# Kernel optimization log

Hardware: AMD Instinct MI355X
Metric: run time of the kernel (lower is better)

The kernel has to match this reference:

```python
import jax, jax.numpy as jnp
import numpy as np

NUM_CLASSES = 19
PROJ_DIM = 128
QUEUE_LEN = 2975
B, H, W = 8, 128, 128
EPS = 1e-12  # torch F.normalize eps


def setup_inputs() -> dict:
    key = jax.random.key(0)
    k0, k1, k2, k3, k4 = jax.random.split(key, 5)
    proj3 = jax.random.normal(k0, (B, PROJ_DIM, H, W), jnp.float32)
    proj4 = jax.random.normal(k1, (B, PROJ_DIM, H, W), jnp.float32)
    proj5 = jax.random.normal(k2, (B, PROJ_DIM, H, W), jnp.float32)
    logits = jax.random.normal(k3, (B, NUM_CLASSES, H, W), jnp.float32)
    q = jax.random.normal(k4, (3, NUM_CLASSES, PROJ_DIM, QUEUE_LEN), jnp.float32)
    # buffers are L2-normalized along proj_dim at init
    queues = q / jnp.maximum(jnp.linalg.norm(q, axis=2, keepdims=True), EPS)
    return {"proj3": proj3, "proj4": proj4, "proj5": proj5,
            "logits": logits, "queues": queues}


def _region_keys(fea, pred):
    """fea: (D, HW) float, pred: (HW,) int. Masked mean per class, L2-normalized."""
    onehot = (pred[None, :] == jnp.arange(NUM_CLASSES)[:, None]).astype(fea.dtype)  # (C, HW)
    counts = onehot.sum(1)                                   # (C,)
    sums = jnp.einsum('ch,dh->cd', onehot, fea)              # (C, D)
    present = counts > 0
    means = sums / jnp.maximum(counts, 1.0)[:, None]
    keys = means / jnp.maximum(jnp.linalg.norm(means, axis=1, keepdims=True), EPS)
    return keys, present


def _contrast_loss(keys, present, queue):
    """keys: (C, D), queue: (C, D, L) (detached in original). Sum over present classes."""
    q = jax.lax.stop_gradient(queue)
    # (query . queue_col) implemented as elementwise-mul + mean over D in the original
    sim = jnp.einsum('cd,kdl->ckl', keys, q) / PROJ_DIM      # (C, C, L)
    ar = jnp.arange(NUM_CLASSES)
    pos = sim[ar, ar, :]                                     # (C, L)  l_pos per class
    exp_all = jnp.exp(sim)
    s_neg = exp_all.sum(axis=(1, 2)) - exp_all[ar, ar, :].sum(1)  # scalar neg mass per class
    loss_c = -(pos - jnp.log(jnp.exp(pos) + s_neg[:, None])).sum(1) / QUEUE_LEN
    return jnp.where(present, loss_c, 0.0).sum()


def _enqueue(queue, ptr, keys, present):
    """Write key into queue column ptr[c] for present classes, advance ptr by 1."""
    ar = jnp.arange(NUM_CLASSES)
    cur = queue[ar, :, ptr]                                  # (C, D)
    newcol = jnp.where(present[:, None], jax.lax.stop_gradient(keys), cur)
    queue = queue.at[ar, :, ptr].set(newcol)
    ptr = jnp.where(present, (ptr + 1) % QUEUE_LEN, ptr)
    return queue, ptr


def reference(proj3, proj4, proj5, logits, queues):
    pred = jnp.argmax(logits, axis=1).reshape(B, -1)         # (B, HW)
    total = jnp.float32(0.0)
    for pi, projector in enumerate((proj3, proj4, proj5)):
        fea_all = projector.reshape(B, PROJ_DIM, -1)          # (B, D, HW)

        def step(carry, inp):
            queue, ptr, acc = carry
            f, p = inp
            keys, present = _region_keys(f, p)
            acc = acc + _contrast_loss(keys, present, queue)
            queue, ptr = _enqueue(queue, ptr, keys, present)
            return (queue, ptr, acc), None

        init = (queues[pi], jnp.zeros((NUM_CLASSES,), jnp.int32), jnp.float32(0.0))
        (_, _, acc), _ = jax.lax.scan(step, init, (fea_all, pred))
        total = total + acc / B
    return total
```

## Files before the change

### kernel.cpp

```cpp
#include <hip/hip_runtime.h>
#include <stdint.h>

#define NCLS 19
#define PDIM 128
#define QLEN 2975
#define BATCH 8
#define HW 16384
#define ROWS 152
#define ROWS_PAD 160
#define HCHUNK 512

typedef __attribute__((ext_vector_type(8))) short short8;
typedef __attribute__((ext_vector_type(4))) float floatx4;

__device__ __forceinline__ uint16_t f2b(float f) {
    uint32_t u = __float_as_uint(f);
    uint32_t r = (u + 0x7FFFu + ((u >> 16) & 1u)) >> 16;
    return (uint16_t)r;
}

__global__ __launch_bounds__(256)
void k_pred(const float* __restrict__ logits, uint8_t* __restrict__ pred,
            int* __restrict__ counts) {
    __shared__ int cnt[NCLS];
    int tid = threadIdx.x;
    if (tid < NCLS) cnt[tid] = 0;
    __syncthreads();
    int idx = blockIdx.x * 256 + tid;
    int b = idx >> 14, h = idx & (HW - 1);
    const float* base = logits + (size_t)b * NCLS * HW + h;
    float best = base[0];
    int bi = 0;
#pragma unroll
    for (int c = 1; c < NCLS; ++c) {
        float v = base[(size_t)c * HW];
        if (v > best) { best = v; bi = c; }
    }
    pred[idx] = (uint8_t)bi;
    atomicAdd(&cnt[bi], 1);
    __syncthreads();
    if (tid < NCLS) atomicAdd(&counts[b * NCLS + tid], cnt[tid]);
}

__global__ __launch_bounds__(512)
void k_msum(const float* __restrict__ p0, const float* __restrict__ p1,
            const float* __restrict__ p2, const uint8_t* __restrict__ pred,
            float* __restrict__ sums) {
    int chunk = blockIdx.x, b = blockIdx.y, pi = blockIdx.z;
    const float* proj = (pi == 0) ? p0 : (pi == 1) ? p1 : p2;
    int tid = threadIdx.x;
    int wave = tid >> 6, lane = tid & 63;
    int col = lane & 15, g = lane >> 4;
    int d = wave * 16 + col;
    int h0 = chunk * HCHUNK;

    const float* frow = proj + ((size_t)b * PDIM + d) * HW + h0;
    const uint8_t* pr = pred + (size_t)b * HW + h0;

    uint4 va[16], vb[16];
    uint64_t pb[16];
#pragma unroll
    for (int s = 0; s < 16; ++s) {
        int hk = s * 32 + g * 8;
        va[s] = *(const uint4*)(frow + hk);
        vb[s] = *(const uint4*)(frow + hk + 4);
        pb[s] = *(const uint64_t*)(pr + hk);
    }
    __builtin_amdgcn_sched_barrier(0);

    floatx4 acc0 = (floatx4)(0.f);
    floatx4 acc1 = (floatx4)(0.f);

#pragma unroll
    for (int s = 0; s < 16; ++s) {
        union { short8 s8; uint32_t w[4]; } bf;
        bf.w[0] = __builtin_amdgcn_perm(va[s].y, va[s].x, 0x07060302u);
        bf.w[1] = __builtin_amdgcn_perm(va[s].w, va[s].z, 0x07060302u);
        bf.w[2] = __builtin_amdgcn_perm(vb[s].y, vb[s].x, 0x07060302u);
        bf.w[3] = __builtin_amdgcn_perm(vb[s].w, vb[s].z, 0x07060302u);

        union { short8 s8; uint16_t h[8]; } a0, a1;
#pragma unroll
        for (int j = 0; j < 8; ++j) {
            int cb = (int)((pb[s] >> (8 * j)) & 0xFF);
            a0.h[j] = (cb == col)      ? (uint16_t)0x3F80 : (uint16_t)0;
            a1.h[j] = (cb == col + 16) ? (uint16_t)0x3F80 : (uint16_t)0;
        }
        acc0 = __builtin_amdgcn_mfma_f32_16x16x32_bf16(a0.s8, bf.s8, acc0, 0, 0, 0);
        acc1 = __builtin_amdgcn_mfma_f32_16x16x32_bf16(a1.s8, bf.s8, acc1, 0, 0, 0);
    }

    float* sb = sums + (((size_t)pi * BATCH + b) * NCLS) * PDIM + d;
#pragma unroll
    for (int r = 0; r < 4; ++r) {
        int row0 = g * 4 + r;
        atomicAdd(&sb[(size_t)row0 * PDIM], acc0[r]);
        int row1 = 16 + g * 4 + r;
        if (row1 < NCLS) atomicAdd(&sb[(size_t)row1 * PDIM], acc1[r]);
    }
}

__global__ __launch_bounds__(64)
void k_keys(const float* __restrict__ sums, const int* __restrict__ counts,
            uint16_t* __restrict__ keysb) {
    int c = blockIdx.x, b = blockIdx.y, pi = blockIdx.z;
    int lane = threadIdx.x;
    size_t base = (((size_t)pi * BATCH + b) * NCLS + c) * PDIM;
    int cn = counts[b * NCLS + c];
    float cnt = (float)(cn > 0 ? cn : 1);
    float m0 = sums[base + lane] / cnt;
    float m1 = sums[base + lane + 64] / cnt;
    float nr = m0 * m0 + m1 * m1;
    for (int off = 32; off; off >>= 1) nr += __shfl_xor(nr, off);
    float scale = 1.f / fmaxf(sqrtf(nr), 1e-12f);
    size_t bb = ((size_t)pi * ROWS_PAD + b * NCLS + c) * PDIM;
    keysb[bb + lane]      = f2b(m0 * scale);
    keysb[bb + lane + 64] = f2b(m1 * scale);
}

__global__ __launch_bounds__(256, 2)
void k_sim(const float* __restrict__ q, const uint16_t* __restrict__ keysb,
           float* __restrict__ Sall, float* __restrict__ D0,
           float* __restrict__ pos0) {
    __shared__ char smem[40960];
    int tile = blockIdx.x, k = blockIdx.y, pi = blockIdx.z;
    int tid = threadIdx.x;
    int wave = tid >> 6, lane = tid & 63;
    int col = lane & 15, g = lane >> 4;

    {
        const uint4* kg = (const uint4*)(keysb + (size_t)pi * ROWS_PAD * PDIM);
        uint4* kl = (uint4*)smem;
        int kgrp = tid & 15;
        int r0 = tid >> 4;
#pragma unroll
        for (int it = 0; it < 10; ++it) {
            int row = r0 + it * 16;
            kl[kgrp * 160 + (row ^ (kgrp & 7))] = kg[row * 16 + kgrp];
        }
    }

    int l0 = tile * 128 + wave * 16 + col;
    int l1 = l0 + 64;
    bool okA = l0 < QLEN, okB = l1 < QLEN;
    const uint32_t* qbase = (const uint32_t*)(q + ((size_t)pi * NCLS + k) * (size_t)PDIM * QLEN);
    const uint32_t* qA = qbase + (okA ? l0 : (QLEN - 1));
    const uint32_t* qB = qbase + (okB ? l1 : (QLEN - 1));

    uint32_t uA[32], uB[32];
#pragma unroll
    for (int s = 0; s < 4; ++s) {
#pragma unroll
        for (int j = 0; j < 8; ++j) {
            size_t off = (size_t)(s * 32 + g * 8 + j) * QLEN;
            uA[s * 8 + j] = qA[off];
            uB[s * 8 + j] = qB[off];
        }
    }

    __syncthreads();

    uint32_t wA[16], wB[16];
#pragma unroll
    for (int t = 0; t < 16; ++t) {
        wA[t] = __builtin_amdgcn_perm(uA[2 * t + 1], uA[2 * t], 0x07060302u);
        wB[t] = __builtin_amdgcn_perm(uB[2 * t + 1], uB[2 * t], 0x07060302u);
    }

    floatx4 accA[10], accB[10];
#pragma unroll
    for (int m = 0; m < 10; ++m) { accA[m] = (floatx4)(0.f); accB[m] = (floatx4)(0.f); }

    const short8* kls = (const short8*)smem;
#pragma unroll
    for (int s = 0; s < 4; ++s) {
        union { short8 s8; uint32_t w[4]; } bfA, bfB;
#pragma unroll
        for (int i = 0; i < 4; ++i) { bfA.w[i] = wA[s * 4 + i]; bfB.w[i] = wB[s * 4 + i]; }
        int kgrp = s * 4 + g;
        int kxor = kgrp & 7;
        const short8* kp = kls + (size_t)kgrp * 160;
#pragma unroll
        for (int m = 0; m < 10; ++m) {
            short8 af = kp[(m * 16 + col) ^ kxor];
            accA[m] = __builtin_amdgcn_mfma_f32_16x16x32_bf16(af, bfA.s8, accA[m], 0, 0, 0);
            accB[m] = __builtin_amdgcn_mfma_f32_16x16x32_bf16(af, bfB.s8, accB[m], 0, 0, 0);
        }
    }

    __syncthreads();
    float* rowsum = (float*)smem;
    if (tid < ROWS_PAD) rowsum[tid] = 0.f;
    __syncthreads();

    const float inv = 1.f / (float)PDIM;
#pragma unroll
    for (int m = 0; m < 10; ++m) {
#pragma unroll
        for (int r = 0; r < 4; ++r) {
            int row = m * 16 + g * 4 + r;
            bool rok = row < ROWS;
            float sA = accA[m][r] * inv;
            float sB = accB[m][r] * inv;
            float e = 0.f;
            if (rok) e = (okA ? __expf(sA) : 0.f) + (okB ? __expf(sB) : 0.f);
#pragma unroll
            for (int off = 1; off < 16; off <<= 1) e += __shfl_xor(e, off);
            if (col == 0 && rok) atomicAdd(&rowsum[row], e);
            if (rok) {
                int bb = row / NCLS, cc = row - bb * NCLS;
                if (cc == k) {
                    float* pb = pos0 + (((size_t)pi * BATCH + bb) * NCLS + cc) * QLEN;
                    if (okA) pb[l0] = sA;
                    if (okB) pb[l1] = sB;
                }
            }
        }
    }
    __syncthreads();
    if (tid < ROWS) {
        float v = rowsum[tid];
        atomicAdd(&Sall[pi * ROWS + tid], v);
        int cc = tid % NCLS;
        if (cc == k) atomicAdd(&D0[pi * ROWS + tid], v);
    }
}

__global__ __launch_bounds__(256)
void k_loss(const float* __restrict__ pos0, const float* __restrict__ Sall,
            const float* __restrict__ D0, const int* __restrict__ counts,
            float* __restrict__ out) {
    int c = blockIdx.x, b = blockIdx.y, pi = blockIdx.z;
    if (counts[b * NCLS + c] <= 0) return;
    int tid = threadIdx.x;
    int row = b * NCLS + c;
    float sneg = Sall[pi * ROWS + row] - D0[pi * ROWS + row];
    const float* pp = pos0 + (((size_t)pi * BATCH + b) * NCLS + c) * QLEN;
    float sum = 0.f;
    for (int l = tid; l < QLEN; l += 256) {
        float p = pp[l];
        sum += p - logf(__expf(p) + sneg);
    }
    __shared__ float red[4];
    int wave = tid >> 6, lane = tid & 63;
    for (int off = 32; off; off >>= 1) sum += __shfl_down(sum, off);
    if (lane == 0) red[wave] = sum;
    __syncthreads();
    if (tid == 0) {
        float t = red[0] + red[1] + red[2] + red[3];
        atomicAdd(out, -t / ((float)QLEN * (float)BATCH));
    }
}

extern "C" void kernel_launch(void* const* d_in, const int* in_sizes, int n_in,
                              void* d_out, int out_size, void* d_ws, size_t ws_size,
                              hipStream_t stream) {
    const float* proj3  = (const float*)d_in[0];
    const float* proj4  = (const float*)d_in[1];
    const float* proj5  = (const float*)d_in[2];
    const float* logits = (const float*)d_in[3];
    const float* queues = (const float*)d_in[4];

    char* ws = (char*)d_ws;
    int*      counts = (int*)ws;
    uint8_t*  pred   = (uint8_t*)(ws + 1024);
    float*    sums   = (float*)(ws + 1024 + 131072);
    uint16_t* keysb  = (uint16_t*)(ws + 365568);
    float*    Sall   = (float*)(ws + 488448);
    float*    D0f    = (float*)(ws + 490496);
    float*    pos0   = (float*)(ws + 492544);

    hipMemsetAsync(ws, 0, 492544, stream);
    hipMemsetAsync(d_out, 0, sizeof(float), stream);

    k_pred<<<dim3(512), 256, 0, stream>>>(logits, pred, counts);

    dim3 gs(32, BATCH, 3);
    k_msum<<<gs, 512, 0, stream>>>(proj3, proj4, proj5, pred, sums);

    dim3 gk(NCLS, BATCH, 3);
    k_keys<<<gk, 64, 0, stream>>>(sums, counts, keysb);

    dim3 gm((QLEN + 127) / 128, NCLS, 3);
    k_sim<<<gm, 256, 0, stream>>>(queues, keysb, Sall, D0f, pos0);

    dim3 gl(NCLS, BATCH, 3);
    k_loss<<<gl, 256, 0, stream>>>(pos0, Sall, D0f, counts, (float*)d_out);
}
```

Baseline: 133.9 us.

## Coalesce projector loads via LDS transpose with double-buffered sub-chunks in k_msum

Restructures the masked-sum kernel so each wave loads whole 512-byte contiguous row segments across lanes, instead of each lane striding through its own feature row. The data is converted to bf16 and transposed through swizzled LDS into MFMA operand layout. The 512-pixel chunk is processed as four 128-pixel sub-chunks with register double-buffering so the next loads overlap the current MFMAs. Launch bounds now request two blocks per CU. This adds LDS traffic and a read-after-write dependency within each wave, and fewer loads are in flight per sub-step than before.

```diff
diff --git a/kernel.cpp b/kernel.cpp
--- a/kernel.cpp
+++ b/kernel.cpp
@@ -8,7 +8,7 @@
 #define HW 16384
 #define ROWS 152
 #define ROWS_PAD 160
-#define HCHUNK 512
+#define NSUB 4
 
 typedef __attribute__((ext_vector_type(8))) short short8;
 typedef __attribute__((ext_vector_type(4))) float floatx4;
@@ -42,55 +42,78 @@
     if (tid < NCLS) atomicAdd(&counts[b * NCLS + tid], cnt[tid]);
 }
 
-__global__ __launch_bounds__(512)
+__global__ __launch_bounds__(512, 2)
 void k_msum(const float* __restrict__ p0, const float* __restrict__ p1,
             const float* __restrict__ p2, const uint8_t* __restrict__ pred,
             float* __restrict__ sums) {
+    __shared__ short lds[8][16][128];
     int chunk = blockIdx.x, b = blockIdx.y, pi = blockIdx.z;
     const float* proj = (pi == 0) ? p0 : (pi == 1) ? p1 : p2;
     int tid = threadIdx.x;
     int wave = tid >> 6, lane = tid & 63;
     int col = lane & 15, g = lane >> 4;
-    int d = wave * 16 + col;
-    int h0 = chunk * HCHUNK;
-
-    const float* frow = proj + ((size_t)b * PDIM + d) * HW + h0;
+    int lo = lane & 31, hi = lane >> 5;
+    int d0 = wave * 16;
+    int h0 = chunk * (128 * NSUB);
+
+    const float* fbase = proj + ((size_t)b * PDIM + d0) * HW + h0;
     const uint8_t* pr = pred + (size_t)b * HW + h0;
-
-    uint4 va[16], vb[16];
-    uint64_t pb[16];
-#pragma unroll
-    for (int s = 0; s < 16; ++s) {
-        int hk = s * 32 + g * 8;
-        va[s] = *(const uint4*)(frow + hk);
-        vb[s] = *(const uint4*)(frow + hk + 4);
-        pb[s] = *(const uint64_t*)(pr + hk);
-    }
-    __builtin_amdgcn_sched_barrier(0);
+    char* wlds = (char*)&lds[wave][0][0];
+
+    uint4 fa[2][8];
+    uint64_t fp[2][4];
+#pragma unroll
+    for (int i = 0; i < 8; ++i)
+        fa[0][i] = *(const uint4*)(fbase + (size_t)(i * 2 + hi) * HW + lo * 4);
+#pragma unroll
+    for (int s = 0; s < 4; ++s)
+        fp[0][s] = *(const uint64_t*)(pr + s * 32 + g * 8);
 
     floatx4 acc0 = (floatx4)(0.f);
     floatx4 acc1 = (floatx4)(0.f);
 
 #pragma unroll
-    for (int s = 0; s < 16; ++s) {
-        union { short8 s8; uint32_t w[4]; } bf;
-        bf.w[0] = __builtin_amdgcn_perm(va[s].y, va[s].x, 0x07060302u);
-        bf.w[1] = __builtin_amdgcn_perm(va[s].w, va[s].z, 0x07060302u);
-        bf.w[2] = __builtin_amdgcn_perm(vb[s].y, vb[s].x, 0x07060302u);
-        bf.w[3] = __builtin_amdgcn_perm(vb[s].w, vb[s].z, 0x07060302u);
-
-        union { short8 s8; uint16_t h[8]; } a0, a1;
-#pragma unroll
-        for (int j = 0; j < 8; ++j) {
-            int cb = (int)((pb[s] >> (8 * j)) & 0xFF);
-            a0.h[j] = (cb == col)      ? (uint16_t)0x3F80 : (uint16_t)0;
-            a1.h[j] = (cb == col + 16) ? (uint16_t)0x3F80 : (uint16_t)0;
-        }
-        acc0 = __builtin_amdgcn_mfma_f32_16x16x32_bf16(a0.s8, bf.s8, acc0, 0, 0, 0);
-        acc1 = __builtin_amdgcn_mfma_f32_16x16x32_bf16(a1.s8, bf.s8, acc1, 0, 0, 0);
-    }
-
-    float* sb = sums + (((size_t)pi * BATCH + b) * NCLS) * PDIM + d;
+    for (int sub = 0; sub < NSUB; ++sub) {
+        int cur = sub & 1, nxt = cur ^ 1;
+        if (sub + 1 < NSUB) {
+            const float* fb = fbase + (sub + 1) * 128;
+            const uint8_t* pn = pr + (sub + 1) * 128;
+#pragma unroll
+            for (int i = 0; i < 8; ++i)
+                fa[nxt][i] = *(const uint4*)(fb + (size_t)(i * 2 + hi) * HW + lo * 4);
+#pragma unroll
+            for (int s = 0; s < 4; ++s)
+                fp[nxt][s] = *(const uint64_t*)(pn + s * 32 + g * 8);
+        }
+        __builtin_amdgcn_sched_barrier(0);
+
+#pragma unroll
+        for (int i = 0; i < 8; ++i) {
+            int r = i * 2 + hi;
+            uint2 w;
+            w.x = __builtin_amdgcn_perm(fa[cur][i].y, fa[cur][i].x, 0x07060302u);
+            w.y = __builtin_amdgcn_perm(fa[cur][i].w, fa[cur][i].z, 0x07060302u);
+            int byte = (r * 256 + lo * 8) ^ ((r & 7) << 4);
+            *(uint2*)(wlds + byte) = w;
+        }
+
+#pragma unroll
+        for (int s = 0; s < 4; ++s) {
+            int byte = (col * 256 + s * 64 + g * 16) ^ ((col & 7) << 4);
+            short8 bf = *(const short8*)(wlds + byte);
+            union { short8 s8; uint16_t h[8]; } a0, a1;
+#pragma unroll
+            for (int j = 0; j < 8; ++j) {
+                int cb = (int)((fp[cur][s] >> (8 * j)) & 0xFF);
+                a0.h[j] = (cb == col)      ? (uint16_t)0x3F80 : (uint16_t)0;
+                a1.h[j] = (cb == col + 16) ? (uint16_t)0x3F80 : (uint16_t)0;
+            }
+            acc0 = __builtin_amdgcn_mfma_f32_16x16x32_bf16(a0.s8, bf, acc0, 0, 0, 0);
+            acc1 = __builtin_amdgcn_mfma_f32_16x16x32_bf16(a1.s8, bf, acc1, 0, 0, 0);
+        }
+    }
+
+    float* sb = sums + (((size_t)pi * BATCH + b) * NCLS) * PDIM + d0 + col;
 #pragma unroll
     for (int r = 0; r < 4; ++r) {
         int row0 = g * 4 + r;
@@ -275,7 +298,7 @@
 
     k_pred<<<dim3(512), 256, 0, stream>>>(logits, pred, counts);
 
-    dim3 gs(32, BATCH, 3);
+    dim3 gs(HW / (128 * NSUB), BATCH, 3);
     k_msum<<<gs, 512, 0, stream>>>(proj3, proj4, proj5, pred, sums);
 
     dim3 gk(NCLS, BATCH, 3);
```

Measured after the change: 128.0 us. 1.05x faster.

## Restage masked-sum loads through swizzled LDS with double-buffered register prefetch

Applied to the files above, without the earlier changes.

The masked-sum kernel now has each block cover 16 feature rows and half of the spatial range. It loads fully coalesced row-contiguous float4s, converts them to bf16 and writes them into a swizzled LDS tile. The next 2048-column stage is prefetched into registers while MFMAs consume the current tile, replacing the earlier strided 8-float per-lane reads. The grid shrinks to 384 blocks, each doing more work. This trades extra LDS traffic and block barriers for better global coalescing, and leaves fewer blocks to hide latency.

```diff
diff --git a/kernel.cpp b/kernel.cpp
--- a/kernel.cpp
+++ b/kernel.cpp
@@ -8,7 +8,6 @@
 #define HW 16384
 #define ROWS 152
 #define ROWS_PAD 160
-#define HCHUNK 512
 
 typedef __attribute__((ext_vector_type(8))) short short8;
 typedef __attribute__((ext_vector_type(4))) float floatx4;
@@ -42,55 +41,92 @@
     if (tid < NCLS) atomicAdd(&counts[b * NCLS + tid], cnt[tid]);
 }
 
-__global__ __launch_bounds__(512)
+__global__ __launch_bounds__(512, 4)
 void k_msum(const float* __restrict__ p0, const float* __restrict__ p1,
             const float* __restrict__ p2, const uint8_t* __restrict__ pred,
             float* __restrict__ sums) {
-    int chunk = blockIdx.x, b = blockIdx.y, pi = blockIdx.z;
+    __shared__ short lds[16][2048];
+    int dg = blockIdx.x >> 1, hh = blockIdx.x & 1;
+    int b = blockIdx.y, pi = blockIdx.z;
     const float* proj = (pi == 0) ? p0 : (pi == 1) ? p1 : p2;
     int tid = threadIdx.x;
     int wave = tid >> 6, lane = tid & 63;
     int col = lane & 15, g = lane >> 4;
-    int d = wave * 16 + col;
-    int h0 = chunk * HCHUNK;
-
-    const float* frow = proj + ((size_t)b * PDIM + d) * HW + h0;
-    const uint8_t* pr = pred + (size_t)b * HW + h0;
-
-    uint4 va[16], vb[16];
-    uint64_t pb[16];
-#pragma unroll
-    for (int s = 0; s < 16; ++s) {
-        int hk = s * 32 + g * 8;
-        va[s] = *(const uint4*)(frow + hk);
-        vb[s] = *(const uint4*)(frow + hk + 4);
-        pb[s] = *(const uint64_t*)(pr + hk);
-    }
-    __builtin_amdgcn_sched_barrier(0);
+
+    const float* fbase = proj + ((size_t)(b * PDIM + dg * 16)) * HW + hh * 8192;
+    const uint8_t* pbase = pred + (size_t)b * HW + hh * 8192;
+    char* ldsb = (char*)&lds[0][0];
+
+    uint4 u[16];
+    uint64_t pb[8];
+
+#pragma unroll
+    for (int i = 0; i < 16; ++i) {
+        int row = 2 * wave + (i >> 3);
+        u[i] = *(const uint4*)(fbase + (size_t)row * HW + (i & 7) * 256 + lane * 4);
+    }
+#pragma unroll
+    for (int i = 0; i < 16; ++i) {
+        int row = 2 * wave + (i >> 3);
+        uint2 w;
+        w.x = __builtin_amdgcn_perm(u[i].y, u[i].x, 0x07060302u);
+        w.y = __builtin_amdgcn_perm(u[i].w, u[i].z, 0x07060302u);
+        int byte = (row * 4096 + (i & 7) * 512 + lane * 8) ^ ((row & 15) << 4);
+        *(uint2*)(ldsb + byte) = w;
+    }
+    __syncthreads();
 
     floatx4 acc0 = (floatx4)(0.f);
     floatx4 acc1 = (floatx4)(0.f);
 
 #pragma unroll
-    for (int s = 0; s < 16; ++s) {
-        union { short8 s8; uint32_t w[4]; } bf;
-        bf.w[0] = __builtin_amdgcn_perm(va[s].y, va[s].x, 0x07060302u);
-        bf.w[1] = __builtin_amdgcn_perm(va[s].w, va[s].z, 0x07060302u);
-        bf.w[2] = __builtin_amdgcn_perm(vb[s].y, vb[s].x, 0x07060302u);
-        bf.w[3] = __builtin_amdgcn_perm(vb[s].w, vb[s].z, 0x07060302u);
-
-        union { short8 s8; uint16_t h[8]; } a0, a1;
-#pragma unroll
-        for (int j = 0; j < 8; ++j) {
-            int cb = (int)((pb[s] >> (8 * j)) & 0xFF);
-            a0.h[j] = (cb == col)      ? (uint16_t)0x3F80 : (uint16_t)0;
-            a1.h[j] = (cb == col + 16) ? (uint16_t)0x3F80 : (uint16_t)0;
-        }
-        acc0 = __builtin_amdgcn_mfma_f32_16x16x32_bf16(a0.s8, bf.s8, acc0, 0, 0, 0);
-        acc1 = __builtin_amdgcn_mfma_f32_16x16x32_bf16(a1.s8, bf.s8, acc1, 0, 0, 0);
-    }
-
-    float* sb = sums + (((size_t)pi * BATCH + b) * NCLS) * PDIM + d;
+    for (int st = 0; st < 4; ++st) {
+#pragma unroll
+        for (int t = 0; t < 8; ++t) {
+            int kk = wave * 8 + t;
+            pb[t] = *(const uint64_t*)(pbase + st * 2048 + kk * 32 + g * 8);
+        }
+        if (st + 1 < 4) {
+#pragma unroll
+            for (int i = 0; i < 16; ++i) {
+                int row = 2 * wave + (i >> 3);
+                u[i] = *(const uint4*)(fbase + (size_t)row * HW +
+                                       (st + 1) * 2048 + (i & 7) * 256 + lane * 4);
+            }
+        }
+        __builtin_amdgcn_sched_barrier(0);
+
+#pragma unroll
+        for (int t = 0; t < 8; ++t) {
+            int kk = wave * 8 + t;
+            int byte = (col * 4096 + kk * 64 + g * 16) ^ ((col & 15) << 4);
+            short8 bf = *(const short8*)(ldsb + byte);
+            union { short8 s8; uint16_t h[8]; } a0, a1;
+#pragma unroll
+            for (int j = 0; j < 8; ++j) {
+                int cb = (int)((pb[t] >> (8 * j)) & 0xFF);
+                a0.h[j] = (cb == col)      ? (uint16_t)0x3F80 : (uint16_t)0;
+                a1.h[j] = (cb == col + 16) ? (uint16_t)0x3F80 : (uint16_t)0;
+            }
+            acc0 = __builtin_amdgcn_mfma_f32_16x16x32_bf16(a0.s8, bf, acc0, 0, 0, 0);
+            acc1 = __builtin_amdgcn_mfma_f32_16x16x32_bf16(a1.s8, bf, acc1, 0, 0, 0);
+        }
+        __syncthreads();
+        if (st + 1 < 4) {
+#pragma unroll
+            for (int i = 0; i < 16; ++i) {
+                int row = 2 * wave + (i >> 3);
+                uint2 w;
+                w.x = __builtin_amdgcn_perm(u[i].y, u[i].x, 0x07060302u);
+                w.y = __builtin_amdgcn_perm(u[i].w, u[i].z, 0x07060302u);
+                int byte = (row * 4096 + (i & 7) * 512 + lane * 8) ^ ((row & 15) << 4);
+                *(uint2*)(ldsb + byte) = w;
+            }
+            __syncthreads();
+        }
+    }
+
+    float* sb = sums + (((size_t)pi * BATCH + b) * NCLS) * PDIM + dg * 16 + col;
 #pragma unroll
     for (int r = 0; r < 4; ++r) {
         int row0 = g * 4 + r;
@@ -275,7 +311,7 @@
 
     k_pred<<<dim3(512), 256, 0, stream>>>(logits, pred, counts);
 
-    dim3 gs(32, BATCH, 3);
+    dim3 gs(16, BATCH, 3);
     k_msum<<<gs, 512, 0, stream>>>(proj3, proj4, proj5, pred, sums);
 
     dim3 gk(NCLS, BATCH, 3);
```

Result: slower. 161.0 us (+20.2%).
